# Kernel tuning notes

Hardware: AMD Instinct MI355X
Metric: run time of the kernel (lower is better)

The kernel has to match this reference:

```python
import jax, jax.numpy as jnp
import numpy as np

EPS = 1e-7  # keras.backend.epsilon()
ROUTINGS = 3


def squash(s, axis=-1):
    # standard capsule squash: ||s||^2/(1+||s||^2) * s/||s||
    n2 = jnp.sum(jnp.square(s), axis=axis, keepdims=True)
    return s * (n2 / (1.0 + n2)) / jnp.sqrt(n2 + EPS)


def setup_inputs() -> dict:
    key = jax.random.key(0)
    k1, k2 = jax.random.split(key)
    B, I, K = 32, 2048, 8          # batch, input capsules, input capsule dim
    J, D = 32, 16                  # output capsules (num_capsules), dim_capsules
    x = jax.random.normal(k1, (B, I, K), dtype=jnp.float32)
    # add_weight with random_normal_initializer(stddev=0.1), shape [J, I, D, K]
    W = 0.1 * jax.random.normal(k2, (J, I, D, K), dtype=jnp.float32)
    return {"x": x, "W": W}


def reference(x, W):
    # u_ji_hat[b,j,i,d] = sum_k W[j,i,d,k] * x[b,i,k]  (the map_fn batched matmul)
    u_hat = jnp.einsum('jidk,bik->bjid', W, x)  # [B, J, I, D]
    B, J, I, D = u_hat.shape
    b = jnp.zeros((B, J, I), dtype=u_hat.dtype)  # routing logits b_ij
    v = None
    for r in range(ROUTINGS):
        c = jax.nn.softmax(b, axis=1)                 # softmax over output capsules J
        s = jnp.einsum('bji,bjid->bjd', c, u_hat)     # weighted sum over input caps i
        v = squash(s, axis=-1)                        # squash over capsule dim (axis=-2 pre-squeeze)
        if r < ROUTINGS - 1:
            # agreement = u_hat^T v : sum over capsule dim d
            b = b + jnp.einsum('bjid,bjd->bji', u_hat, v)
    return v  # [B, J, D] == tf.squeeze(v_j, [2, 4])
```

## Files before the change

kernel.cpp:

```cpp
#include <hip/hip_runtime.h>
#include <hip/hip_fp16.h>


#define ICAP    2048
#define JD      512
#define S_ELEMS 16384
#define EPSQ    1e-7f
#define NBP     256
#define ICH     8

#if defined(__has_builtin) && __has_builtin(__builtin_amdgcn_rcpf)
#define FAST_RCP(x) __builtin_amdgcn_rcpf(x)
#else
#define FAST_RCP(x) (1.0f / (x))
#endif
#if defined(__has_builtin) && __has_builtin(__builtin_amdgcn_rsqf)
#define FAST_RSQ(x) __builtin_amdgcn_rsqf(x)
#else
#define FAST_RSQ(x) rsqrtf(x)
#endif

__global__ __launch_bounds__(256)
void caps_transpose(const float4* __restrict__ Wv, float4* __restrict__ Wt) {
    __shared__ float4 buf[16 * 66];
    const int i = blockIdx.x;
    const int t = threadIdx.x;
#pragma unroll
    for (int q = 0; q < 4; ++q) {
        const int f = q * 256 + t;
        const int jj = f >> 5, c = f & 31;
        buf[(c & 15) * 66 + 2 * jj + (c >> 4)] =
            Wv[(size_t)jj * 65536 + (size_t)i * 32 + c];
    }
    __syncthreads();
    float4* dst = Wt + (size_t)i * 1024;
#pragma unroll
    for (int q = 0; q < 4; ++q) {
        const int o = q * 256 + t;
        dst[o] = buf[(o >> 6) * 66 + (o & 63)];
    }
}

__global__ __launch_bounds__(512, 1)
void caps_pass(const float4* __restrict__ Wt, const float* __restrict__ x,
               const float* __restrict__ vsum, __half* __restrict__ partials) {
    const int tid  = threadIdx.x;
    const int wave = tid >> 6;
    const int lane = tid & 63;
    const int j    = lane & 31;
    const int dh   = lane >> 5;
    const int i0   = blockIdx.x * ICH;

    float vs[4][8], sacc[4][8];
#pragma unroll
    for (int bb = 0; bb < 4; ++bb) {
        const int b = wave + 8 * bb;
        const float* vp = vsum + b * JD + j * 16 + dh * 8;
        float4 a  = *reinterpret_cast<const float4*>(vp);
        float4 bq = *reinterpret_cast<const float4*>(vp + 4);
        vs[bb][0]=a.x; vs[bb][1]=a.y; vs[bb][2]=a.z; vs[bb][3]=a.w;
        vs[bb][4]=bq.x; vs[bb][5]=bq.y; vs[bb][6]=bq.z; vs[bb][7]=bq.w;
#pragma unroll
        for (int r = 0; r < 8; ++r) sacc[bb][r] = 0.f;
    }

    const float4* wp = Wt + (size_t)i0 * 1024 + 2 * j + dh;

#pragma unroll 1
    for (int il = 0; il < ICH; ++il) {
        float4 w4[16];
#pragma unroll
        for (int cc = 0; cc < 16; ++cc)
            w4[cc] = wp[(size_t)il * 1024 + cc * 64];

        const int gi = i0 + il;
#pragma unroll
        for (int bb = 0; bb < 4; ++bb) {
            const int b = wave + 8 * bb;
            const float* xp = x + ((size_t)b * ICAP + gi) * 8;
            const float4 x0 = *reinterpret_cast<const float4*>(xp);
            const float4 x1 = *reinterpret_cast<const float4*>(xp + 4);

            float u[8], tpart = 0.f;
#pragma unroll
            for (int r = 0; r < 8; ++r) {
                const float4 wa = w4[2 * r], wb = w4[2 * r + 1];
                float acc;
                acc = wa.x * x0.x;
                acc = fmaf(wa.y, x0.y, acc);
                acc = fmaf(wa.z, x0.z, acc);
                acc = fmaf(wa.w, x0.w, acc);
                acc = fmaf(wb.x, x1.x, acc);
                acc = fmaf(wb.y, x1.y, acc);
                acc = fmaf(wb.z, x1.z, acc);
                acc = fmaf(wb.w, x1.w, acc);
                u[r] = acc;
                tpart = fmaf(acc, vs[bb][r], tpart);
            }
            const float t = tpart + __shfl_xor(tpart, 32);
            const float e = __expf(t);
            float se = e;
#pragma unroll
            for (int off = 1; off <= 16; off <<= 1)
                se += __shfl_xor(se, off);
            const float c = e * FAST_RCP(se);
#pragma unroll
            for (int r = 0; r < 8; ++r)
                sacc[bb][r] = fmaf(c, u[r], sacc[bb][r]);
        }
    }

    __half* pout = partials + (size_t)blockIdx.x * S_ELEMS;
#pragma unroll
    for (int bb = 0; bb < 4; ++bb) {
        const int b = wave + 8 * bb;
        union { int4 v; __half2 h[4]; } pk;
#pragma unroll
        for (int r = 0; r < 4; ++r)
            pk.h[r] = __floats2half2_rn(sacc[bb][2 * r], sacc[bb][2 * r + 1]);
        *reinterpret_cast<int4*>(pout + b * JD + j * 16 + dh * 8) = pk.v;
    }
}

__global__ __launch_bounds__(1024)
void caps_reduce(const __half* __restrict__ partials, float* __restrict__ vsum,
                 float* __restrict__ out) {
    __shared__ float buf[16][80];
    const int tid = threadIdx.x;
    const int eL  = tid & 63;
    const int sg  = tid >> 6;
    const int e   = blockIdx.x * 64 + eL;

    float s = 0.f;
    const __half* p = partials + (size_t)sg * S_ELEMS + e;
#pragma unroll
    for (int n = 0; n < 16; ++n)
        s += __half2float(p[(size_t)(n * 16) * S_ELEMS]);
    buf[sg][eL] = s;
    __syncthreads();

    if (sg == 0) {
        s = 0.f;
#pragma unroll
        for (int k = 0; k < 16; ++k) s += buf[k][eL];
        float n2 = s * s;
#pragma unroll
        for (int off = 1; off <= 8; off <<= 1)
            n2 += __shfl_xor(n2, off);
        const float scale = n2 * FAST_RCP(1.f + n2) * FAST_RSQ(n2 + EPSQ);
        const float v = s * scale;
        vsum[e] += v;
        if (out) out[e] = v;
    }
}

extern "C" void kernel_launch(void* const* d_in, const int* in_sizes, int n_in,
                              void* d_out, int out_size, void* d_ws, size_t ws_size,
                              hipStream_t stream) {
    const float* x = (const float*)d_in[0];
    const float* W = (const float*)d_in[1];
    float* out = (float*)d_out;

    float4* Wt       = (float4*)d_ws;
    float*  vsum     = (float*)((char*)d_ws + (size_t)ICAP * 1024 * 16);
    __half* partials = (__half*)((char*)vsum + S_ELEMS * sizeof(float));

    hipMemsetAsync(vsum, 0, S_ELEMS * sizeof(float), stream);
    caps_transpose<<<ICAP, 256, 0, stream>>>((const float4*)W, Wt);

    for (int r = 0; r < 3; ++r) {
        caps_pass<<<NBP, 512, 0, stream>>>(Wt, x, vsum, partials);
        caps_reduce<<<S_ELEMS / 64, 1024, 0, stream>>>(
            partials, vsum, (r == 2) ? out : nullptr);
    }
}
```

Before: 176.3 us.

## Store W and x in fp16, use fdot2, specialize first routing pass

The prep kernel now converts W to fp16 while transposing it and also converts x to fp16, which halves the bytes each routing pass reads. The inner products use packed fp16 dot2 instructions with fp32 accumulation. A templated first pass skips the softmax and agreement math because the coefficients are uniform, and the memset is replaced by a first-pass flag in the reduce kernel. Rounding W and x to fp16 adds error to the results, and the transposing write through shared memory is replaced by direct scattered stores.

```diff
diff --git a/kernel.cpp b/kernel.cpp
--- a/kernel.cpp
+++ b/kernel.cpp
@@ -9,6 +9,16 @@
 #define NBP     256
 #define ICH     8
 
+typedef _Float16 h2v __attribute__((ext_vector_type(2)));
+union H8 { int4 i4; h2v h[4]; };
+
+#if defined(__has_builtin) && __has_builtin(__builtin_amdgcn_fdot2)
+#define FDOT2(a, b, c) __builtin_amdgcn_fdot2((a), (b), (c), false)
+#else
+__device__ inline float FDOT2(h2v a, h2v b, float c) {
+    return c + (float)a[0] * (float)b[0] + (float)a[1] * (float)b[1];
+}
+#endif
 #if defined(__has_builtin) && __has_builtin(__builtin_amdgcn_rcpf)
 #define FAST_RCP(x) __builtin_amdgcn_rcpf(x)
 #else
@@ -21,28 +31,31 @@
 #endif
 
 __global__ __launch_bounds__(256)
-void caps_transpose(const float4* __restrict__ Wv, float4* __restrict__ Wt) {
-    __shared__ float4 buf[16 * 66];
+void caps_prep(const float4* __restrict__ Wv, const float* __restrict__ x,
+               ushort4* __restrict__ Wt, __half* __restrict__ xh) {
     const int i = blockIdx.x;
     const int t = threadIdx.x;
 #pragma unroll
     for (int q = 0; q < 4; ++q) {
-        const int f = q * 256 + t;
+        const int f  = q * 256 + t;
         const int jj = f >> 5, c = f & 31;
-        buf[(c & 15) * 66 + 2 * jj + (c >> 4)] =
-            Wv[(size_t)jj * 65536 + (size_t)i * 32 + c];
+        const float4 w = Wv[(size_t)jj * 65536 + (size_t)i * 32 + c];
+        ushort4 h;
+        h.x = __half_as_ushort(__float2half(w.x));
+        h.y = __half_as_ushort(__float2half(w.y));
+        h.z = __half_as_ushort(__float2half(w.z));
+        h.w = __half_as_ushort(__float2half(w.w));
+        const int dh = c >> 4, cc = (c & 15) >> 1, sub = c & 1;
+        Wt[((size_t)i * 512 + cc * 64 + 2 * jj + dh) * 2 + sub] = h;
     }
-    __syncthreads();
-    float4* dst = Wt + (size_t)i * 1024;
-#pragma unroll
-    for (int q = 0; q < 4; ++q) {
-        const int o = q * 256 + t;
-        dst[o] = buf[(o >> 6) * 66 + (o & 63)];
-    }
+    const int b = t >> 3, k = t & 7;
+    const size_t xi = ((size_t)b * ICAP + i) * 8 + k;
+    xh[xi] = __float2half(x[xi]);
 }
 
+template <int FIRST>
 __global__ __launch_bounds__(512, 1)
-void caps_pass(const float4* __restrict__ Wt, const float* __restrict__ x,
+void caps_pass(const int4* __restrict__ Wt, const int4* __restrict__ xh,
                const float* __restrict__ vsum, __half* __restrict__ partials) {
     const int tid  = threadIdx.x;
     const int wave = tid >> 6;
@@ -55,55 +68,55 @@
 #pragma unroll
     for (int bb = 0; bb < 4; ++bb) {
         const int b = wave + 8 * bb;
-        const float* vp = vsum + b * JD + j * 16 + dh * 8;
-        float4 a  = *reinterpret_cast<const float4*>(vp);
-        float4 bq = *reinterpret_cast<const float4*>(vp + 4);
-        vs[bb][0]=a.x; vs[bb][1]=a.y; vs[bb][2]=a.z; vs[bb][3]=a.w;
-        vs[bb][4]=bq.x; vs[bb][5]=bq.y; vs[bb][6]=bq.z; vs[bb][7]=bq.w;
+        if (!FIRST) {
+            const float* vp = vsum + b * JD + j * 16 + dh * 8;
+            const float4 a  = *reinterpret_cast<const float4*>(vp);
+            const float4 bq = *reinterpret_cast<const float4*>(vp + 4);
+            vs[bb][0]=a.x; vs[bb][1]=a.y; vs[bb][2]=a.z; vs[bb][3]=a.w;
+            vs[bb][4]=bq.x; vs[bb][5]=bq.y; vs[bb][6]=bq.z; vs[bb][7]=bq.w;
+        }
 #pragma unroll
         for (int r = 0; r < 8; ++r) sacc[bb][r] = 0.f;
     }
 
-    const float4* wp = Wt + (size_t)i0 * 1024 + 2 * j + dh;
+    const int4* wp = Wt + (size_t)i0 * 512 + 2 * j + dh;
 
-#pragma unroll 1
+#pragma unroll
     for (int il = 0; il < ICH; ++il) {
-        float4 w4[16];
+        H8 w8[8];
 #pragma unroll
-        for (int cc = 0; cc < 16; ++cc)
-            w4[cc] = wp[(size_t)il * 1024 + cc * 64];
+        for (int cc = 0; cc < 8; ++cc)
+            w8[cc].i4 = wp[(size_t)il * 512 + cc * 64];
 
         const int gi = i0 + il;
 #pragma unroll
         for (int bb = 0; bb < 4; ++bb) {
             const int b = wave + 8 * bb;
-            const float* xp = x + ((size_t)b * ICAP + gi) * 8;
-            const float4 x0 = *reinterpret_cast<const float4*>(xp);
-            const float4 x1 = *reinterpret_cast<const float4*>(xp + 4);
+            H8 xv;
+            xv.i4 = xh[(size_t)b * ICAP + gi];
 
             float u[8], tpart = 0.f;
 #pragma unroll
             for (int r = 0; r < 8; ++r) {
-                const float4 wa = w4[2 * r], wb = w4[2 * r + 1];
-                float acc;
-                acc = wa.x * x0.x;
-                acc = fmaf(wa.y, x0.y, acc);
-                acc = fmaf(wa.z, x0.z, acc);
-                acc = fmaf(wa.w, x0.w, acc);
-                acc = fmaf(wb.x, x1.x, acc);
-                acc = fmaf(wb.y, x1.y, acc);
-                acc = fmaf(wb.z, x1.z, acc);
-                acc = fmaf(wb.w, x1.w, acc);
+                float acc = FDOT2(w8[r].h[0], xv.h[0], 0.f);
+                acc = FDOT2(w8[r].h[1], xv.h[1], acc);
+                acc = FDOT2(w8[r].h[2], xv.h[2], acc);
+                acc = FDOT2(w8[r].h[3], xv.h[3], acc);
                 u[r] = acc;
-                tpart = fmaf(acc, vs[bb][r], tpart);
+                if (!FIRST) tpart = fmaf(acc, vs[bb][r], tpart);
             }
-            const float t = tpart + __shfl_xor(tpart, 32);
-            const float e = __expf(t);
-            float se = e;
+            float c;
+            if (FIRST) {
+                c = 0.03125f;
+            } else {
+                const float t = tpart + __shfl_xor(tpart, 32);
+                const float e = __expf(t);
+                float se = e;
 #pragma unroll
-            for (int off = 1; off <= 16; off <<= 1)
-                se += __shfl_xor(se, off);
-            const float c = e * FAST_RCP(se);
+                for (int off = 1; off <= 16; off <<= 1)
+                    se += __shfl_xor(se, off);
+                c = e * FAST_RCP(se);
+            }
 #pragma unroll
             for (int r = 0; r < 8; ++r)
                 sacc[bb][r] = fmaf(c, u[r], sacc[bb][r]);
@@ -124,7 +137,7 @@
 
 __global__ __launch_bounds__(1024)
 void caps_reduce(const __half* __restrict__ partials, float* __restrict__ vsum,
-                 float* __restrict__ out) {
+                 float* __restrict__ out, int first) {
     __shared__ float buf[16][80];
     const int tid = threadIdx.x;
     const int eL  = tid & 63;
@@ -149,7 +162,8 @@
             n2 += __shfl_xor(n2, off);
         const float scale = n2 * FAST_RCP(1.f + n2) * FAST_RSQ(n2 + EPSQ);
         const float v = s * scale;
-        vsum[e] += v;
+        const float old = first ? 0.f : vsum[e];
+        vsum[e] = old + v;
         if (out) out[e] = v;
     }
 }
@@ -161,16 +175,22 @@
     const float* W = (const float*)d_in[1];
     float* out = (float*)d_out;
 
-    float4* Wt       = (float4*)d_ws;
-    float*  vsum     = (float*)((char*)d_ws + (size_t)ICAP * 1024 * 16);
-    __half* partials = (__half*)((char*)vsum + S_ELEMS * sizeof(float));
+    ushort4* Wt      = (ushort4*)d_ws;
+    __half*  xh      = (__half*)((char*)d_ws + (size_t)ICAP * 512 * 16);
+    float*   vsum    = (float*)((char*)xh + (size_t)32 * ICAP * 8 * 2);
+    __half*  partials= (__half*)((char*)vsum + S_ELEMS * sizeof(float));
 
-    hipMemsetAsync(vsum, 0, S_ELEMS * sizeof(float), stream);
-    caps_transpose<<<ICAP, 256, 0, stream>>>((const float4*)W, Wt);
+    caps_prep<<<ICAP, 256, 0, stream>>>((const float4*)W, x, Wt, xh);
 
-    for (int r = 0; r < 3; ++r) {
-        caps_pass<<<NBP, 512, 0, stream>>>(Wt, x, vsum, partials);
-        caps_reduce<<<S_ELEMS / 64, 1024, 0, stream>>>(
-            partials, vsum, (r == 2) ? out : nullptr);
-    }
+    caps_pass<1><<<NBP, 512, 0, stream>>>((const int4*)Wt, (const int4*)xh,
+                                          vsum, partials);
+    caps_reduce<<<S_ELEMS / 64, 1024, 0, stream>>>(partials, vsum, nullptr, 1);
+
+    caps_pass<0><<<NBP, 512, 0, stream>>>((const int4*)Wt, (const int4*)xh,
+                                          vsum, partials);
+    caps_reduce<<<S_ELEMS / 64, 1024, 0, stream>>>(partials, vsum, nullptr, 0);
+
+    caps_pass<0><<<NBP, 512, 0, stream>>>((const int4*)Wt, (const int4*)xh,
+                                          vsum, partials);
+    caps_reduce<<<S_ELEMS / 64, 1024, 0, stream>>>(partials, vsum, out, 0);
 }
```

New measurement: 160.0 us. 9.2% less time.
